# Optimization experiments

Measured on AMD Instinct MI355X. Metric: run time of the kernel, lower is better.

## Reference

```python
import jax, jax.numpy as jnp
import numpy as np

H, KV, D, EPS = 32, 8, 128, 1e-6
G = H // KV  # kv groups = 4
ROPE_THETA = 5000000.0


def _rms_norm(x, gamma):
    # x: (..., D)
    return x * jax.lax.rsqrt(jnp.mean(x * x, axis=-1, keepdims=True) + EPS) * gamma


def _rotate_half(x):
    x1, x2 = jnp.split(x, 2, axis=-1)
    return jnp.concatenate([-x2, x1], axis=-1)


def _apply_rope(x, cos, sin):
    # x: (b, h, s, D); cos/sin: (b, s, 1, D) -> (b, 1, s, D)
    cos = jnp.transpose(cos, (0, 2, 1, 3))
    sin = jnp.transpose(sin, (0, 2, 1, 3))
    return x * cos + _rotate_half(x) * sin


def setup_inputs() -> dict:
    key = jax.random.key(0)
    ks = jax.random.split(key, 8)
    b, s, hid = 2, 2048, 2560
    hidden = jax.random.normal(ks[0], (b, s, hid), dtype=jnp.float32)
    # realistic RoPE tables (half-split convention matching _rotate_half)
    inv_freq = 1.0 / (ROPE_THETA ** (np.arange(0, D, 2, dtype=np.float32) / D))  # (D/2,)
    pos = np.arange(s, dtype=np.float32)
    freqs = np.outer(pos, inv_freq)                     # (s, D/2)
    emb = np.concatenate([freqs, freqs], axis=-1)       # (s, D)
    cos = jnp.broadcast_to(jnp.asarray(np.cos(emb))[None, :, None, :], (b, s, 1, D))
    sin = jnp.broadcast_to(jnp.asarray(np.sin(emb))[None, :, None, :], (b, s, 1, D))
    sc = 1.0 / np.sqrt(hid)
    wq = jax.random.normal(ks[1], (H * D, hid), dtype=jnp.float32) * sc
    wk = jax.random.normal(ks[2], (KV * D, hid), dtype=jnp.float32) * sc
    wv = jax.random.normal(ks[3], (KV * D, hid), dtype=jnp.float32) * sc
    wo = jax.random.normal(ks[4], (hid, H * D), dtype=jnp.float32) * (1.0 / np.sqrt(H * D))
    q_gamma = jnp.ones((D,), dtype=jnp.float32)
    k_gamma = jnp.ones((D,), dtype=jnp.float32)
    return {"hidden": hidden, "cos": cos, "sin": sin, "wq": wq, "wk": wk,
            "wv": wv, "wo": wo, "q_gamma": q_gamma, "k_gamma": k_gamma}


def reference(hidden, cos, sin, wq, wk, wv, wo, q_gamma, k_gamma):
    b, s, _ = hidden.shape
    # projections -> (b, heads, s, D)
    q = (hidden @ wq.T).reshape(b, s, H, D).transpose(0, 2, 1, 3)
    k = (hidden @ wk.T).reshape(b, s, KV, D).transpose(0, 2, 1, 3)
    v = (hidden @ wv.T).reshape(b, s, KV, D).transpose(0, 2, 1, 3)
    # QK-RMSNorm over head_dim
    q = _rms_norm(q, q_gamma)
    k = _rms_norm(k, k_gamma)
    # RoPE
    q = _apply_rope(q, cos, sin)
    k = _apply_rope(k, cos, sin)
    new_k, new_v = k, v  # kv cache (no prior cache)
    # GQA attention without materializing expanded K/V
    qg = q.reshape(b, KV, G, s, D)
    scale = 1.0 / np.sqrt(D)
    scores = jnp.einsum('bkgqd,bkld->bkgql', qg, k) * scale  # (b,KV,G,s,s)
    causal = jnp.tril(jnp.ones((s, s), dtype=bool))
    scores = jnp.where(causal, scores, jnp.finfo(scores.dtype).min)
    probs = jax.nn.softmax(scores, axis=-1)
    out = jnp.einsum('bkgql,bkld->bkgqd', probs, v)          # (b,KV,G,s,D)
    out = out.reshape(b, H, s, D).transpose(0, 2, 1, 3).reshape(b, s, H * D)
    return (out @ wo.T, new_k, new_v)
```

## Files before the change

kernel.cpp:

```cpp
#include <hip/hip_runtime.h>
#include <stdint.h>

typedef unsigned short u16;
typedef __attribute__((ext_vector_type(8))) short short8;
typedef __attribute__((ext_vector_type(4))) float f32x4;

#define MFMA_BF16(a,b,c) __builtin_amdgcn_mfma_f32_16x16x32_bf16((a),(b),(c),0,0,0)

__device__ __forceinline__ u16 f2bf(float x) {
    uint32_t u = __builtin_bit_cast(uint32_t, x);
    u += 0x7fffu + ((u >> 16) & 1u);
    return (u16)(u >> 16);
}
__device__ __forceinline__ float bf2f(u16 u) {
    return __builtin_bit_cast(float, (uint32_t)u << 16);
}
__device__ __forceinline__ void glds16(const void* g, void* lds) {
    __builtin_amdgcn_global_load_lds((const __attribute__((address_space(1))) void*)g,
                                     (__attribute__((address_space(3))) void*)lds,
                                     16, 0, 0);
}

__global__ __launch_bounds__(256) void cvt_kernel(const float* __restrict__ src,
                                                  u16* __restrict__ dst, int n) {
    int i = (blockIdx.x * 256 + threadIdx.x) * 4;
    if (i + 4 <= n) {
        float4 v = *(const float4*)(src + i);
        ushort4 o;
        o.x = f2bf(v.x); o.y = f2bf(v.y); o.z = f2bf(v.z); o.w = f2bf(v.w);
        *(ushort4*)(dst + i) = o;
    }
}

template<bool BF16_OUT>
__global__ __launch_bounds__(256) void gemm_bt(const u16* __restrict__ A,
                                               const u16* __restrict__ B,
                                               void* __restrict__ Cv,
                                               int K, int lda, int ldb, int ldc)
{
    __shared__ __align__(16) u16 As[128 * 32];
    __shared__ __align__(16) u16 Bs[128 * 32];
    const int t = threadIdx.x;
    const int w = t >> 6, l = t & 63;
    const int m0 = blockIdx.y * 128, n0 = blockIdx.x * 128;
    const int wm = (w & 1) * 64, wn = (w >> 1) * 64;
    const int lrow = l & 15, lk = l >> 4;

    f32x4 acc[4][4];
#pragma unroll
    for (int i = 0; i < 4; i++)
#pragma unroll
        for (int j = 0; j < 4; j++) acc[i][j] = (f32x4){0.f, 0.f, 0.f, 0.f};

    const int c0 = t, c1 = t + 256;
    const int r0 = c0 >> 2, g0 = (c0 & 3) ^ ((r0 >> 1) & 3);
    const int r1 = c1 >> 2, g1 = (c1 & 3) ^ ((r1 >> 1) & 3);
    const u16* Ap0 = A + (size_t)(m0 + r0) * lda + g0 * 8;
    const u16* Ap1 = A + (size_t)(m0 + r1) * lda + g1 * 8;
    const u16* Bp0 = B + (size_t)(n0 + r0) * ldb + g0 * 8;
    const u16* Bp1 = B + (size_t)(n0 + r1) * ldb + g1 * 8;
    char* Asb = (char*)As + w * 1024;
    char* Bsb = (char*)Bs + w * 1024;

    for (int k0 = 0; k0 < K; k0 += 32) {
        __syncthreads();
        glds16(Ap0 + k0, Asb);
        glds16(Ap1 + k0, Asb + 4096);
        glds16(Bp0 + k0, Bsb);
        glds16(Bp1 + k0, Bsb + 4096);
        __syncthreads();
        short8 af[4], bf[4];
#pragma unroll
        for (int mi = 0; mi < 4; mi++) {
            int r = wm + mi * 16 + lrow;
            int sl = lk ^ ((r >> 1) & 3);
            af[mi] = *(const short8*)&As[r * 32 + sl * 8];
        }
#pragma unroll
        for (int ni = 0; ni < 4; ni++) {
            int r = wn + ni * 16 + lrow;
            int sl = lk ^ ((r >> 1) & 3);
            bf[ni] = *(const short8*)&Bs[r * 32 + sl * 8];
        }
#pragma unroll
        for (int mi = 0; mi < 4; mi++)
#pragma unroll
            for (int ni = 0; ni < 4; ni++)
                acc[mi][ni] = MFMA_BF16(af[mi], bf[ni], acc[mi][ni]);
    }

#pragma unroll
    for (int mi = 0; mi < 4; mi++) {
#pragma unroll
        for (int r = 0; r < 4; r++) {
            int row = m0 + wm + mi * 16 + lk * 4 + r;
#pragma unroll
            for (int ni = 0; ni < 4; ni++) {
                int col = n0 + wn + ni * 16 + lrow;
                float v = acc[mi][ni][r];
                if (BF16_OUT) ((u16*)Cv)[(size_t)row * ldc + col] = f2bf(v);
                else          ((float*)Cv)[(size_t)row * ldc + col] = v;
            }
        }
    }
}

__global__ __launch_bounds__(256) void norm_rope(const u16* __restrict__ qkv,
        const float* __restrict__ cosb, const float* __restrict__ sinb,
        const float* __restrict__ qg, const float* __restrict__ kg,
        u16* __restrict__ qb, u16* __restrict__ kb, u16* __restrict__ vtb,
        float* __restrict__ k_out, float* __restrict__ v_out)
{
    const int idx = blockIdx.x * 4 + (threadIdx.x >> 6);
    const int l = threadIdx.x & 63;
    const int tok = idx / 48, hd = idx - tok * 48;
    const int b = tok >> 11, pos = tok & 2047;
    const u16* row = qkv + (size_t)tok * 6144 + hd * 128;
    float x1 = bf2f(row[l]), x2 = bf2f(row[l + 64]);
    float ss = x1 * x1 + x2 * x2;
#pragma unroll
    for (int m = 1; m < 64; m <<= 1) ss += __shfl_xor(ss, m, 64);
    float rn = rsqrtf(ss * (1.0f / 128.0f) + 1e-6f);

    if (hd < 40) {
        const float* gm = (hd < 32) ? qg : kg;
        float xn1 = x1 * rn * gm[l];
        float xn2 = x2 * rn * gm[l + 64];
        float c1 = cosb[(size_t)tok * 128 + l],      s1 = sinb[(size_t)tok * 128 + l];
        float c2 = cosb[(size_t)tok * 128 + l + 64], s2 = sinb[(size_t)tok * 128 + l + 64];
        float y1 = xn1 * c1 - xn2 * s1;
        float y2 = xn2 * c2 + xn1 * s2;
        if (hd < 32) {
            const float qs = 0.08838834764831845f;
            size_t base = (((size_t)b * 32 + hd) * 2048 + pos) * 128;
            qb[base + l]      = f2bf(y1 * qs);
            qb[base + l + 64] = f2bf(y2 * qs);
        } else {
            int kv = hd - 32;
            size_t base = (((size_t)b * 8 + kv) * 2048 + pos) * 128;
            k_out[base + l] = y1; k_out[base + l + 64] = y2;
            kb[base + l] = f2bf(y1); kb[base + l + 64] = f2bf(y2);
        }
    } else {
        int kv = hd - 40;
        size_t base = (((size_t)b * 8 + kv) * 2048 + pos) * 128;
        v_out[base + l] = x1; v_out[base + l + 64] = x2;
        size_t tbase = ((size_t)b * 8 + kv) * 128;
        vtb[(tbase + l) * 2048 + pos]      = f2bf(x1);
        vtb[(tbase + l + 64) * 2048 + pos] = f2bf(x2);
    }
}

__global__ __launch_bounds__(256) void attn_kernel(const u16* __restrict__ qb,
        const u16* __restrict__ kb, const u16* __restrict__ vtb,
        u16* __restrict__ ao)
{
    __shared__ __align__(16) u16 Ks[64 * 128];
    __shared__ __align__(16) u16 Vs[128 * 64];
    __shared__ __align__(16) u16 Ps[4][16 * 72];

    const int bh = blockIdx.x;
    const int b = bh >> 5, h = bh & 31;
    const int kvh = h >> 2;
    const int qt = blockIdx.y;
    const int q0 = qt * 64;
    const int t = threadIdx.x, w = t >> 6, l = t & 63;
    const int lrow = l & 15, lk = l >> 4;

    const u16* qbase  = qb  + ((size_t)b * 32 + h)  * 2048 * 128;
    const u16* kbase  = kb  + ((size_t)b * 8 + kvh) * 2048 * 128;
    const u16* vtbase = vtb + ((size_t)b * 8 + kvh) * 128 * 2048;

    short8 qf[4];
    {
        const u16* qrow = qbase + (size_t)(q0 + w * 16 + lrow) * 128 + lk * 8;
#pragma unroll
        for (int ks = 0; ks < 4; ks++) qf[ks] = *(const short8*)(qrow + ks * 32);
    }

    f32x4 o[8];
#pragma unroll
    for (int i = 0; i < 8; i++) o[i] = (f32x4){0.f, 0.f, 0.f, 0.f};
    float mprev[4], lsum[4];
#pragma unroll
    for (int r = 0; r < 4; r++) { mprev[r] = -1e30f; lsum[r] = 0.f; }

    int kR[4], kG[4], vR[4], vG[4];
#pragma unroll
    for (int i = 0; i < 4; i++) {
        int c = i * 256 + t;
        kR[i] = c >> 4; kG[i] = (c & 15) ^ (kR[i] & 7);
        vR[i] = c >> 3; vG[i] = (c & 7)  ^ (vR[i] & 7);
    }
    char* Ksb = (char*)Ks + w * 1024;
    char* Vsb = (char*)Vs + w * 1024;
    u16* pw = &Ps[w][0];

    for (int kt = 0; kt <= qt; kt++) {
        const int kv0 = kt * 64;
        __syncthreads();
#pragma unroll
        for (int i = 0; i < 4; i++)
            glds16(kbase + (size_t)(kv0 + kR[i]) * 128 + kG[i] * 8, Ksb + i * 4096);
#pragma unroll
        for (int i = 0; i < 4; i++)
            glds16(vtbase + (size_t)vR[i] * 2048 + kv0 + vG[i] * 8, Vsb + i * 4096);
        __syncthreads();

        f32x4 s[4];
#pragma unroll
        for (int i = 0; i < 4; i++) s[i] = (f32x4){0.f, 0.f, 0.f, 0.f};
#pragma unroll
        for (int ks = 0; ks < 4; ks++) {
#pragma unroll
            for (int nt = 0; nt < 4; nt++) {
                int r = nt * 16 + lrow;
                int sl = (ks * 4 + lk) ^ (r & 7);
                short8 kf = *(const short8*)&Ks[r * 128 + sl * 8];
                s[nt] = MFMA_BF16(qf[ks], kf, s[nt]);
            }
        }

        if (kt == qt) {
#pragma unroll
            for (int nt = 0; nt < 4; nt++) {
                int cg = kv0 + nt * 16 + lrow;
#pragma unroll
                for (int r = 0; r < 4; r++) {
                    int rg = q0 + w * 16 + lk * 4 + r;
                    if (cg > rg) s[nt][r] = -1e30f;
                }
            }
        }

        float mnew[4], alpha[4], rs[4];
#pragma unroll
        for (int r = 0; r < 4; r++) {
            float mx = fmaxf(fmaxf(s[0][r], s[1][r]), fmaxf(s[2][r], s[3][r]));
            mx = fmaxf(mx, __shfl_xor(mx, 1, 64));
            mx = fmaxf(mx, __shfl_xor(mx, 2, 64));
            mx = fmaxf(mx, __shfl_xor(mx, 4, 64));
            mx = fmaxf(mx, __shfl_xor(mx, 8, 64));
            mnew[r] = fmaxf(mprev[r], mx);
            alpha[r] = __expf(mprev[r] - mnew[r]);
            mprev[r] = mnew[r];
            rs[r] = 0.f;
        }
#pragma unroll
        for (int nt = 0; nt < 4; nt++)
#pragma unroll
            for (int r = 0; r < 4; r++) {
                float p = __expf(s[nt][r] - mnew[r]);
                s[nt][r] = p;
                rs[r] += p;
            }
#pragma unroll
        for (int r = 0; r < 4; r++) {
            rs[r] += __shfl_xor(rs[r], 1, 64);
            rs[r] += __shfl_xor(rs[r], 2, 64);
            rs[r] += __shfl_xor(rs[r], 4, 64);
            rs[r] += __shfl_xor(rs[r], 8, 64);
            lsum[r] = lsum[r] * alpha[r] + rs[r];
        }
#pragma unroll
        for (int i = 0; i < 8; i++)
#pragma unroll
            for (int r = 0; r < 4; r++) o[i][r] *= alpha[r];

#pragma unroll
        for (int nt = 0; nt < 4; nt++)
#pragma unroll
            for (int r = 0; r < 4; r++)
                pw[(lk * 4 + r) * 72 + nt * 16 + lrow] = f2bf(s[nt][r]);
        asm volatile("s_waitcnt lgkmcnt(0)" ::: "memory");

#pragma unroll
        for (int k2 = 0; k2 < 2; k2++) {
            short8 pf = *(const short8*)&pw[lrow * 72 + k2 * 32 + lk * 8];
#pragma unroll
            for (int nt = 0; nt < 8; nt++) {
                int r = nt * 16 + lrow;
                int sl = (k2 * 4 + lk) ^ (r & 7);
                short8 vf = *(const short8*)&Vs[r * 64 + sl * 8];
                o[nt] = MFMA_BF16(pf, vf, o[nt]);
            }
        }
    }

    float inv[4];
#pragma unroll
    for (int r = 0; r < 4; r++) inv[r] = 1.0f / lsum[r];
#pragma unroll
    for (int nt = 0; nt < 8; nt++)
#pragma unroll
        for (int r = 0; r < 4; r++) {
            int tok = q0 + w * 16 + lk * 4 + r;
            size_t off = ((size_t)b * 2048 + tok) * 4096 + h * 128 + nt * 16 + lrow;
            ao[off] = f2bf(o[nt][r] * inv[r]);
        }
}

extern "C" void kernel_launch(void* const* d_in, const int* in_sizes, int n_in,
                              void* d_out, int out_size, void* d_ws, size_t ws_size,
                              hipStream_t stream)
{
    (void)in_sizes; (void)n_in; (void)out_size; (void)ws_size;
    const float* hidden = (const float*)d_in[0];
    const float* cosb   = (const float*)d_in[1];
    const float* sinb   = (const float*)d_in[2];
    const float* wq     = (const float*)d_in[3];
    const float* wk     = (const float*)d_in[4];
    const float* wv     = (const float*)d_in[5];
    const float* wo     = (const float*)d_in[6];
    const float* qg     = (const float*)d_in[7];
    const float* kg     = (const float*)d_in[8];

    float* out   = (float*)d_out;
    float* k_out = out + (size_t)2 * 2048 * 2560;
    float* v_out = k_out + (size_t)2 * 8 * 2048 * 128;

    u16* hid_b = (u16*)d_ws;
    u16* w_b   = hid_b + 10485760;
    u16* wo_b  = w_b   + 15728640;
    u16* q_b   = wo_b  + 10485760;
    u16* k_b   = q_b   + 16777216;
    u16* vt_b  = k_b   + 4194304;
    u16* qkv_b = vt_b  + 4194304;
    u16* ao_b  = hid_b;

    cvt_kernel<<<10240, 256, 0, stream>>>(hidden, hid_b, 10485760);
    cvt_kernel<<<10240, 256, 0, stream>>>(wq, w_b, 10485760);
    cvt_kernel<<<2560,  256, 0, stream>>>(wk, w_b + 10485760, 2621440);
    cvt_kernel<<<2560,  256, 0, stream>>>(wv, w_b + 13107200, 2621440);
    cvt_kernel<<<10240, 256, 0, stream>>>(wo, wo_b, 10485760);

    gemm_bt<true><<<dim3(48, 32), 256, 0, stream>>>(hid_b, w_b, qkv_b,
                                                    2560, 2560, 2560, 6144);
    norm_rope<<<49152, 256, 0, stream>>>(qkv_b, cosb, sinb, qg, kg,
                                         q_b, k_b, vt_b, k_out, v_out);
    attn_kernel<<<dim3(64, 32), 256, 0, stream>>>(q_b, k_b, vt_b, ao_b);
    gemm_bt<false><<<dim3(20, 32), 256, 0, stream>>>(ao_b, wo_b, out,
                                                     4096, 4096, 4096, 2560);
}
```

Measured before the change: 741.1 us.

## Tile attention at 128 query rows, drop running max, and transpose V through LDS

The attention kernel now gives each warp two 16-row query fragments, so each block covers 128 query rows and reuses every loaded K/V tile twice as often. Blocks are launched heaviest causal tile first, and warps skip fully masked tiles. Softmax drops the running-max rescale and exponentiates raw scores, which relies on QK-RMSNorm keeping scores small; a large gamma could overflow this. The V transpose moves out of norm_rope into a separate LDS-tiled kernel, replacing the strided 2-byte scattered stores with coalesced vector writes.

```diff
diff --git a/kernel.cpp b/kernel.cpp
--- a/kernel.cpp
+++ b/kernel.cpp
@@ -105,15 +105,14 @@
     }
 }
 
-__global__ __launch_bounds__(256) void norm_rope(const u16* __restrict__ qkv,
+__global__ __launch_bounds__(256) void norm_rope_qk(const u16* __restrict__ qkv,
         const float* __restrict__ cosb, const float* __restrict__ sinb,
         const float* __restrict__ qg, const float* __restrict__ kg,
-        u16* __restrict__ qb, u16* __restrict__ kb, u16* __restrict__ vtb,
-        float* __restrict__ k_out, float* __restrict__ v_out)
+        u16* __restrict__ qb, u16* __restrict__ kb, float* __restrict__ k_out)
 {
     const int idx = blockIdx.x * 4 + (threadIdx.x >> 6);
     const int l = threadIdx.x & 63;
-    const int tok = idx / 48, hd = idx - tok * 48;
+    const int tok = idx / 40, hd = idx - tok * 40;
     const int b = tok >> 11, pos = tok & 2047;
     const u16* row = qkv + (size_t)tok * 6144 + hd * 128;
     float x1 = bf2f(row[l]), x2 = bf2f(row[l + 64]);
@@ -122,48 +121,77 @@
     for (int m = 1; m < 64; m <<= 1) ss += __shfl_xor(ss, m, 64);
     float rn = rsqrtf(ss * (1.0f / 128.0f) + 1e-6f);
 
-    if (hd < 40) {
-        const float* gm = (hd < 32) ? qg : kg;
-        float xn1 = x1 * rn * gm[l];
-        float xn2 = x2 * rn * gm[l + 64];
-        float c1 = cosb[(size_t)tok * 128 + l],      s1 = sinb[(size_t)tok * 128 + l];
-        float c2 = cosb[(size_t)tok * 128 + l + 64], s2 = sinb[(size_t)tok * 128 + l + 64];
-        float y1 = xn1 * c1 - xn2 * s1;
-        float y2 = xn2 * c2 + xn1 * s2;
-        if (hd < 32) {
-            const float qs = 0.08838834764831845f;
-            size_t base = (((size_t)b * 32 + hd) * 2048 + pos) * 128;
-            qb[base + l]      = f2bf(y1 * qs);
-            qb[base + l + 64] = f2bf(y2 * qs);
-        } else {
-            int kv = hd - 32;
-            size_t base = (((size_t)b * 8 + kv) * 2048 + pos) * 128;
-            k_out[base + l] = y1; k_out[base + l + 64] = y2;
-            kb[base + l] = f2bf(y1); kb[base + l + 64] = f2bf(y2);
-        }
+    const float* gm = (hd < 32) ? qg : kg;
+    float xn1 = x1 * rn * gm[l];
+    float xn2 = x2 * rn * gm[l + 64];
+    float c1 = cosb[(size_t)tok * 128 + l],      s1 = sinb[(size_t)tok * 128 + l];
+    float c2 = cosb[(size_t)tok * 128 + l + 64], s2 = sinb[(size_t)tok * 128 + l + 64];
+    float y1 = xn1 * c1 - xn2 * s1;
+    float y2 = xn2 * c2 + xn1 * s2;
+    if (hd < 32) {
+        const float qs = 0.08838834764831845f;
+        size_t base = (((size_t)b * 32 + hd) * 2048 + pos) * 128;
+        qb[base + l]      = f2bf(y1 * qs);
+        qb[base + l + 64] = f2bf(y2 * qs);
     } else {
-        int kv = hd - 40;
+        int kv = hd - 32;
         size_t base = (((size_t)b * 8 + kv) * 2048 + pos) * 128;
-        v_out[base + l] = x1; v_out[base + l + 64] = x2;
-        size_t tbase = ((size_t)b * 8 + kv) * 128;
-        vtb[(tbase + l) * 2048 + pos]      = f2bf(x1);
-        vtb[(tbase + l + 64) * 2048 + pos] = f2bf(x2);
-    }
-}
-
-__global__ __launch_bounds__(256) void attn_kernel(const u16* __restrict__ qb,
+        k_out[base + l] = y1; k_out[base + l + 64] = y2;
+        kb[base + l] = f2bf(y1); kb[base + l + 64] = f2bf(y2);
+    }
+}
+
+__global__ __launch_bounds__(256) void v_pack(const u16* __restrict__ qkv,
+        float* __restrict__ v_out, u16* __restrict__ vtb)
+{
+    __shared__ __align__(16) u16 T[64 * 128];
+    const int pb = blockIdx.x, bkv = blockIdx.y;
+    const int b = bkv >> 3, kv = bkv & 7;
+    const int p0 = pb * 64;
+    const int t = threadIdx.x;
+    const int pos = t >> 2, ch4 = t & 3;
+    const u16* src = qkv + (size_t)(b * 2048 + p0 + pos) * 6144 + (40 + kv) * 128 + ch4 * 32;
+    float* vdst = v_out + ((size_t)bkv * 2048 + p0 + pos) * 128 + ch4 * 32;
+#pragma unroll
+    for (int j = 0; j < 4; j++) {
+        short8 x = *(const short8*)(src + j * 8);
+        float4 f0, f1;
+        f0.x = bf2f(x[0]); f0.y = bf2f(x[1]); f0.z = bf2f(x[2]); f0.w = bf2f(x[3]);
+        f1.x = bf2f(x[4]); f1.y = bf2f(x[5]); f1.z = bf2f(x[6]); f1.w = bf2f(x[7]);
+        *(float4*)(vdst + j * 8)     = f0;
+        *(float4*)(vdst + j * 8 + 4) = f1;
+        int slot = (ch4 * 4 + j) ^ (pos & 7);
+        *(short8*)&T[pos * 128 + slot * 8] = x;
+    }
+    __syncthreads();
+    const int d = t & 127, ph = t >> 7;
+    u16* obase = vtb + ((size_t)bkv * 128 + d) * 2048 + p0 + ph * 32;
+#pragma unroll
+    for (int g = 0; g < 4; g++) {
+        short8 tv;
+#pragma unroll
+        for (int jj = 0; jj < 8; jj++) {
+            int pp = ph * 32 + g * 8 + jj;
+            int slot = (d >> 3) ^ (pp & 7);
+            tv[jj] = (short)T[pp * 128 + slot * 8 + (d & 7)];
+        }
+        *(short8*)(obase + g * 8) = tv;
+    }
+}
+
+__global__ __launch_bounds__(256, 3) void attn_kernel(const u16* __restrict__ qb,
         const u16* __restrict__ kb, const u16* __restrict__ vtb,
         u16* __restrict__ ao)
 {
     __shared__ __align__(16) u16 Ks[64 * 128];
     __shared__ __align__(16) u16 Vs[128 * 64];
-    __shared__ __align__(16) u16 Ps[4][16 * 72];
+    __shared__ __align__(16) u16 Ps[4][32 * 72];
 
     const int bh = blockIdx.x;
     const int b = bh >> 5, h = bh & 31;
     const int kvh = h >> 2;
-    const int qt = blockIdx.y;
-    const int q0 = qt * 64;
+    const int qt = (int)gridDim.y - 1 - (int)blockIdx.y;
+    const int q0 = qt * 128;
     const int t = threadIdx.x, w = t >> 6, l = t & 63;
     const int lrow = l & 15, lk = l >> 4;
 
@@ -171,19 +199,20 @@
     const u16* kbase  = kb  + ((size_t)b * 8 + kvh) * 2048 * 128;
     const u16* vtbase = vtb + ((size_t)b * 8 + kvh) * 128 * 2048;
 
-    short8 qf[4];
-    {
-        const u16* qrow = qbase + (size_t)(q0 + w * 16 + lrow) * 128 + lk * 8;
-#pragma unroll
-        for (int ks = 0; ks < 4; ks++) qf[ks] = *(const short8*)(qrow + ks * 32);
-    }
-
-    f32x4 o[8];
-#pragma unroll
-    for (int i = 0; i < 8; i++) o[i] = (f32x4){0.f, 0.f, 0.f, 0.f};
-    float mprev[4], lsum[4];
-#pragma unroll
-    for (int r = 0; r < 4; r++) { mprev[r] = -1e30f; lsum[r] = 0.f; }
+    short8 qf[2][4];
+#pragma unroll
+    for (int m = 0; m < 2; m++) {
+        const u16* qrow = qbase + (size_t)(q0 + w * 32 + m * 16 + lrow) * 128 + lk * 8;
+#pragma unroll
+        for (int ks = 0; ks < 4; ks++) qf[m][ks] = *(const short8*)(qrow + ks * 32);
+    }
+
+    f32x4 o[2][8];
+#pragma unroll
+    for (int m = 0; m < 2; m++)
+#pragma unroll
+        for (int i = 0; i < 8; i++) o[m][i] = (f32x4){0.f, 0.f, 0.f, 0.f};
+    float lsum[2][4] = {{0.f,0.f,0.f,0.f},{0.f,0.f,0.f,0.f}};
 
     int kR[4], kG[4], vR[4], vG[4];
 #pragma unroll
@@ -195,8 +224,10 @@
     char* Ksb = (char*)Ks + w * 1024;
     char* Vsb = (char*)Vs + w * 1024;
     u16* pw = &Ps[w][0];
-
-    for (int kt = 0; kt <= qt; kt++) {
+    const int wrow_max = q0 + w * 32 + 31;
+
+    const int nkt = 2 * qt + 2;
+    for (int kt = 0; kt < nkt; kt++) {
         const int kv0 = kt * 64;
         __syncthreads();
 #pragma unroll
@@ -207,9 +238,13 @@
             glds16(vtbase + (size_t)vR[i] * 2048 + kv0 + vG[i] * 8, Vsb + i * 4096);
         __syncthreads();
 
-        f32x4 s[4];
-#pragma unroll
-        for (int i = 0; i < 4; i++) s[i] = (f32x4){0.f, 0.f, 0.f, 0.f};
+        if (kv0 > wrow_max) continue;
+
+        f32x4 s[2][4];
+#pragma unroll
+        for (int m = 0; m < 2; m++)
+#pragma unroll
+            for (int i = 0; i < 4; i++) s[m][i] = (f32x4){0.f, 0.f, 0.f, 0.f};
 #pragma unroll
         for (int ks = 0; ks < 4; ks++) {
 #pragma unroll
@@ -217,87 +252,71 @@
                 int r = nt * 16 + lrow;
                 int sl = (ks * 4 + lk) ^ (r & 7);
                 short8 kf = *(const short8*)&Ks[r * 128 + sl * 8];
-                s[nt] = MFMA_BF16(qf[ks], kf, s[nt]);
-            }
-        }
-
-        if (kt == qt) {
-#pragma unroll
-            for (int nt = 0; nt < 4; nt++) {
-                int cg = kv0 + nt * 16 + lrow;
+                s[0][nt] = MFMA_BF16(qf[0][ks], kf, s[0][nt]);
+                s[1][nt] = MFMA_BF16(qf[1][ks], kf, s[1][nt]);
+            }
+        }
+
+#pragma unroll
+        for (int m = 0; m < 2; m++) {
+            const int rowbase = q0 + w * 32 + m * 16;
+            if (kv0 + 63 > rowbase) {
+#pragma unroll
+                for (int nt = 0; nt < 4; nt++) {
+                    int cg = kv0 + nt * 16 + lrow;
+#pragma unroll
+                    for (int r = 0; r < 4; r++)
+                        if (cg > rowbase + lk * 4 + r) s[m][nt][r] = -1e30f;
+                }
+            }
+#pragma unroll
+            for (int nt = 0; nt < 4; nt++)
 #pragma unroll
                 for (int r = 0; r < 4; r++) {
-                    int rg = q0 + w * 16 + lk * 4 + r;
-                    if (cg > rg) s[nt][r] = -1e30f;
+                    float p = __expf(s[m][nt][r]);
+                    s[m][nt][r] = p;
+                    lsum[m][r] += p;
+                    pw[(m * 16 + lk * 4 + r) * 72 + nt * 16 + lrow] = f2bf(p);
                 }
-            }
-        }
-
-        float mnew[4], alpha[4], rs[4];
+        }
+        asm volatile("s_waitcnt lgkmcnt(0)" ::: "memory");
+
+#pragma unroll
+        for (int k2 = 0; k2 < 2; k2++) {
+            short8 pf0 = *(const short8*)&pw[lrow * 72 + k2 * 32 + lk * 8];
+            short8 pf1 = *(const short8*)&pw[(16 + lrow) * 72 + k2 * 32 + lk * 8];
+#pragma unroll
+            for (int nt = 0; nt < 8; nt++) {
+                int rr = nt * 16 + lrow;
+                int sl = (k2 * 4 + lk) ^ (rr & 7);
+                short8 vf = *(const short8*)&Vs[rr * 64 + sl * 8];
+                o[0][nt] = MFMA_BF16(pf0, vf, o[0][nt]);
+                o[1][nt] = MFMA_BF16(pf1, vf, o[1][nt]);
+            }
+        }
+    }
+
+#pragma unroll
+    for (int m = 0; m < 2; m++)
 #pragma unroll
         for (int r = 0; r < 4; r++) {
-            float mx = fmaxf(fmaxf(s[0][r], s[1][r]), fmaxf(s[2][r], s[3][r]));
-            mx = fmaxf(mx, __shfl_xor(mx, 1, 64));
-            mx = fmaxf(mx, __shfl_xor(mx, 2, 64));
-            mx = fmaxf(mx, __shfl_xor(mx, 4, 64));
-            mx = fmaxf(mx, __shfl_xor(mx, 8, 64));
-            mnew[r] = fmaxf(mprev[r], mx);
-            alpha[r] = __expf(mprev[r] - mnew[r]);
-            mprev[r] = mnew[r];
-            rs[r] = 0.f;
-        }
-#pragma unroll
-        for (int nt = 0; nt < 4; nt++)
+            float v = lsum[m][r];
+            v += __shfl_xor(v, 1, 64);
+            v += __shfl_xor(v, 2, 64);
+            v += __shfl_xor(v, 4, 64);
+            v += __shfl_xor(v, 8, 64);
+            lsum[m][r] = 1.0f / v;
+        }
+#pragma unroll
+    for (int m = 0; m < 2; m++)
+#pragma unroll
+        for (int nt = 0; nt < 8; nt++)
 #pragma unroll
             for (int r = 0; r < 4; r++) {
-                float p = __expf(s[nt][r] - mnew[r]);
-                s[nt][r] = p;
-                rs[r] += p;
-            }
-#pragma unroll
-        for (int r = 0; r < 4; r++) {
-            rs[r] += __shfl_xor(rs[r], 1, 64);
-            rs[r] += __shfl_xor(rs[r], 2, 64);
-            rs[r] += __shfl_xor(rs[r], 4, 64);
-            rs[r] += __shfl_xor(rs[r], 8, 64);
-            lsum[r] = lsum[r] * alpha[r] + rs[r];
-        }
-#pragma unroll
-        for (int i = 0; i < 8; i++)
-#pragma unroll
-            for (int r = 0; r < 4; r++) o[i][r] *= alpha[r];
-
-#pragma unroll
-        for (int nt = 0; nt < 4; nt++)
-#pragma unroll
-            for (int r = 0; r < 4; r++)
-                pw[(lk * 4 + r) * 72 + nt * 16 + lrow] = f2bf(s[nt][r]);
-        asm volatile("s_waitcnt lgkmcnt(0)" ::: "memory");
-
-#pragma unroll
-        for (int k2 = 0; k2 < 2; k2++) {
-            short8 pf = *(const short8*)&pw[lrow * 72 + k2 * 32 + lk * 8];
-#pragma unroll
-            for (int nt = 0; nt < 8; nt++) {
-                int r = nt * 16 + lrow;
-                int sl = (k2 * 4 + lk) ^ (r & 7);
-                short8 vf = *(const short8*)&Vs[r * 64 + sl * 8];
-                o[nt] = MFMA_BF16(pf, vf, o[nt]);
-            }
-        }
-    }
-
-    float inv[4];
-#pragma unroll
-    for (int r = 0; r < 4; r++) inv[r] = 1.0f / lsum[r];
-#pragma unroll
-    for (int nt = 0; nt < 8; nt++)
-#pragma unroll
-        for (int r = 0; r < 4; r++) {
-            int tok = q0 + w * 16 + lk * 4 + r;
-            size_t off = ((size_t)b * 2048 + tok) * 4096 + h * 128 + nt * 16 + lrow;
-            ao[off] = f2bf(o[nt][r] * inv[r]);
-        }
+                int tok = q0 + w * 32 + m * 16 + lk * 4 + r;
+                size_t off = ((size_t)b * 2048 + tok) * 4096 + h * 128 + nt * 16 + lrow;
+                ao[off] = f2bf(o[m][nt][r] * lsum[m][r]);
+            }
 }
 
 extern "C" void kernel_launch(void* const* d_in, const int* in_sizes, int n_in,
@@ -336,9 +355,10 @@
 
     gemm_bt<true><<<dim3(48, 32), 256, 0, stream>>>(hid_b, w_b, qkv_b,
                                                     2560, 2560, 2560, 6144);
-    norm_rope<<<49152, 256, 0, stream>>>(qkv_b, cosb, sinb, qg, kg,
-                                         q_b, k_b, vt_b, k_out, v_out);
-    attn_kernel<<<dim3(64, 32), 256, 0, stream>>>(q_b, k_b, vt_b, ao_b);
+    norm_rope_qk<<<40960, 256, 0, stream>>>(qkv_b, cosb, sinb, qg, kg,
+                                            q_b, k_b, k_out);
+    v_pack<<<dim3(32, 16), 256, 0, stream>>>(qkv_b, v_out, vt_b);
+    attn_kernel<<<dim3(64, 16), 256, 0, stream>>>(q_b, k_b, vt_b, ao_b);
     gemm_bt<false><<<dim3(20, 32), 256, 0, stream>>>(ao_b, wo_b, out,
                                                      4096, 4096, 4096, 2560);
 }
```

New measurement: 674.9 us. 8.9% less time.
